# Kernel tuning notes

Measured on AMD Instinct MI355X. Metric: run time of the kernel, lower is better.

Reference implementation:

```python
import jax, jax.numpy as jnp
import numpy as np

B, S, CIN = 16384, 24, 10
NH, DK, DM = 16, 8, 256
DV = DM // NH  # 16
EPS = 1e-5
T_POS = 1000.0


def _ln(x, g, b):
    mu = jnp.mean(x, axis=-1, keepdims=True)
    var = jnp.mean((x - mu) ** 2, axis=-1, keepdims=True)
    return (x - mu) * jax.lax.rsqrt(var + EPS) * g + b


def _bn(x, g, b, m, v):
    # eval-mode BatchNorm1d over channel (last) dim
    return (x - m) * jax.lax.rsqrt(v + EPS) * g + b


def setup_inputs() -> dict:
    key = jax.random.key(0)
    ks = jax.random.split(key, 16)
    x = jax.random.normal(ks[0], (B, S, CIN + 1), dtype=jnp.float32)
    pos = jax.random.uniform(ks[1], (B, S), dtype=jnp.float32) * 365.0
    x = x.at[:, :, 0].set(pos)
    w = lambda k, shp, s=0.05: (jax.random.normal(k, shp, dtype=jnp.float32) * s)
    d = {
        'x': x,
        'ln1_g': jnp.ones((CIN,), jnp.float32), 'ln1_b': jnp.zeros((CIN,), jnp.float32),
        'conv_w': w(ks[2], (DM, CIN)), 'conv_b': jnp.zeros((DM,), jnp.float32),
        'bn1_g': jnp.ones((DM,), jnp.float32), 'bn1_b': jnp.zeros((DM,), jnp.float32),
        'bn1_m': jnp.zeros((DM,), jnp.float32), 'bn1_v': jnp.ones((DM,), jnp.float32),
        'Q': w(ks[3], (NH, DK), float(np.sqrt(2.0 / DK))),
        'Wk': w(ks[4], (NH * DK, DM), float(np.sqrt(2.0 / DK))), 'bk': jnp.zeros((NH * DK,), jnp.float32),
        'W1': w(ks[5], (128, 256)), 'b1': jnp.zeros((128,), jnp.float32),
        'bn2_g': jnp.ones((128,), jnp.float32), 'bn2_b': jnp.zeros((128,), jnp.float32),
        'bn2_m': jnp.zeros((128,), jnp.float32), 'bn2_v': jnp.ones((128,), jnp.float32),
        'oln_g': jnp.ones((128,), jnp.float32), 'oln_b': jnp.zeros((128,), jnp.float32),
        'Wd1': w(ks[6], (64, 128)), 'bd1': jnp.zeros((64,), jnp.float32),
        'bnd1_g': jnp.ones((64,), jnp.float32), 'bnd1_b': jnp.zeros((64,), jnp.float32),
        'bnd1_m': jnp.zeros((64,), jnp.float32), 'bnd1_v': jnp.ones((64,), jnp.float32),
        'Wd2': w(ks[7], (32, 64)), 'bd2': jnp.zeros((32,), jnp.float32),
        'bnd2_g': jnp.ones((32,), jnp.float32), 'bnd2_b': jnp.zeros((32,), jnp.float32),
        'bnd2_m': jnp.zeros((32,), jnp.float32), 'bnd2_v': jnp.ones((32,), jnp.float32),
        'Wd3': w(ks[8], (20, 32)), 'bd3': jnp.zeros((20,), jnp.float32),
    }
    return d


def reference(x, ln1_g, ln1_b, conv_w, conv_b, bn1_g, bn1_b, bn1_m, bn1_v,
              Q, Wk, bk, W1, b1, bn2_g, bn2_b, bn2_m, bn2_v, oln_g, oln_b,
              Wd1, bd1, bnd1_g, bnd1_b, bnd1_m, bnd1_v,
              Wd2, bd2, bnd2_g, bnd2_b, bnd2_m, bnd2_v, Wd3, bd3):
    pos = x[:, :, 0]            # (B, S) positions
    feat = x[:, :, 1:]          # (B, S, CIN)
    feat = _ln(feat, ln1_g, ln1_b)
    # inconv: 1x1 Conv1d == per-timestep Linear, then eval BatchNorm1d over channels
    h = jnp.einsum('bsc,dc->bsd', feat, conv_w) + conv_b
    h = _bn(h, bn1_g, bn1_b, bn1_m, bn1_v)
    # sinusoid positional encoding, interleaved sin/cos
    div = jnp.exp(jnp.arange(0, DM, 2, dtype=jnp.float32) * (-np.log(T_POS) / DM))  # (DM/2,)
    ang = pos[:, :, None] * div                                   # (B, S, DM/2)
    pe = jnp.stack([jnp.sin(ang), jnp.cos(ang)], axis=-1).reshape(pos.shape[0], pos.shape[1], DM)
    e = h + pe                                                    # (B, S, DM)
    # LTAE multi-head attention with shared learned query
    k = jnp.einsum('bsd,hkd->bshk', e, Wk.reshape(NH, DK, DM)) + bk.reshape(NH, DK)
    logits = jnp.einsum('hk,bshk->bhs', Q, k) / np.sqrt(DK)
    attn = jax.nn.softmax(logits, axis=-1)                        # (B, NH, S); dropout=eval
    v = e.reshape(e.shape[0], e.shape[1], NH, DV)                 # head-chunked values
    o = jnp.einsum('bhs,bshc->bhc', attn, v).reshape(e.shape[0], NH * DV)  # (B, 256)
    # MLP3: Linear(256,128) + BN + ReLU, then dropout(eval) + LayerNorm
    m = jax.nn.relu(_bn(o @ W1.T + b1, bn2_g, bn2_b, bn2_m, bn2_v))
    m = _ln(m, oln_g, oln_b)
    # decoder: [128,64,32,20]
    d1 = jax.nn.relu(_bn(m @ Wd1.T + bd1, bnd1_g, bnd1_b, bnd1_m, bnd1_v))
    d2 = jax.nn.relu(_bn(d1 @ Wd2.T + bd2, bnd2_g, bnd2_b, bnd2_m, bnd2_v))
    out = d2 @ Wd3.T + bd3                                        # (B, 20)
    return out
```

## Files before the change

kernel.cpp:

```cpp
#include <hip/hip_runtime.h>
#include <hip/hip_bf16.h>


typedef __attribute__((ext_vector_type(8))) short bf16x8;
typedef __attribute__((ext_vector_type(4))) float f32x4;

#define EPS 1e-5f
#define INV_SQRT8 0.35355339059327373f
#define KDIV (-0.07785768972392256f)
#define INV2PI 0.15915494309189535f
#define LOG2E 1.4426950408889634f

__device__ __forceinline__ unsigned short f2bf(float f){
  union { float f; unsigned u; } v; v.f = f;
  unsigned r = v.u + 0x7FFFu + ((v.u >> 16) & 1u);
  return (unsigned short)(r >> 16);
}
__device__ __forceinline__ float bf2f(unsigned short h){
  union { unsigned u; float f; } v; v.u = ((unsigned)h) << 16; return v.f;
}
__device__ __forceinline__ unsigned pk2bf(float lo, float hi){
  __hip_bfloat162 h2 = __float22bfloat162_rn(make_float2(lo, hi));
  return *reinterpret_cast<unsigned*>(&h2);
}
__device__ __forceinline__ float sin_rev(float rev){
  rev -= floorf(rev);
  return __builtin_amdgcn_sinf(rev);
}

__global__ __launch_bounds__(256) void k0_pre(
    const float* __restrict__ conv_w, const float* __restrict__ conv_b,
    const float* __restrict__ bn1_g, const float* __restrict__ bn1_b,
    const float* __restrict__ bn1_m, const float* __restrict__ bn1_v,
    const float* __restrict__ Q, const float* __restrict__ Wk,
    const float* __restrict__ bk,
    const float* __restrict__ W1, const float* __restrict__ b1,
    const float* __restrict__ bn2_g, const float* __restrict__ bn2_b,
    const float* __restrict__ bn2_m, const float* __restrict__ bn2_v,
    const float* __restrict__ oln_g, const float* __restrict__ oln_b,
    const float* __restrict__ Wd1, const float* __restrict__ bd1,
    const float* __restrict__ bnd1_g, const float* __restrict__ bnd1_b,
    const float* __restrict__ bnd1_m, const float* __restrict__ bnd1_v,
    const float* __restrict__ Wd2, const float* __restrict__ bd2,
    const float* __restrict__ bnd2_g, const float* __restrict__ bnd2_b,
    const float* __restrict__ bnd2_m, const float* __restrict__ bnd2_v,
    const float* __restrict__ Wd3,
    unsigned short* __restrict__ wqF, unsigned short* __restrict__ w1F,
    unsigned short* __restrict__ wd1F, unsigned short* __restrict__ wd2F,
    unsigned short* __restrict__ wd3F,
    float* __restrict__ convwT, float* __restrict__ convbE,
    float* __restrict__ biasq, float* __restrict__ b1E,
    float* __restrict__ bd1E, float* __restrict__ bd2E)
{
  __shared__ float redL[256];
  const int t = threadIdx.x;
  const int bid = blockIdx.x;

  if (bid < 64){
    for (int e = bid*512 + t; e < bid*512 + 512; e += 256){
      int j = e & 7, lj = (e >> 3) & 63, kc = (e >> 9) & 7, nt = (e >> 12) & 7;
      int n = nt*16 + (lj & 15);
      int k = kc*32 + ((lj >> 4) << 3) + j;
      float s2 = bn2_g[n] * rsqrtf(bn2_v[n] + EPS);
      w1F[e] = f2bf(W1[n*256 + k] * s2);
    }
  } else if (bid < 68){
    int base = (bid - 64)*2048;
    #pragma unroll 4
    for (int it = 0; it < 8; ++it){
      int e = base + it*256 + t;
      int j = e & 7, lj = (e >> 3) & 63, kc = (e >> 9) & 3, nt = (e >> 11) & 3;
      int n = nt*16 + (lj & 15);
      int k = kc*32 + ((lj >> 4) << 3) + j;
      float sd = bnd1_g[n] * rsqrtf(bnd1_v[n] + EPS);
      wd1F[e] = f2bf(Wd1[n*128 + k] * sd * oln_g[k]);
    }
  } else if (bid == 68){
    #pragma unroll 4
    for (int it = 0; it < 8; ++it){
      int e = it*256 + t;
      int j = e & 7, lj = (e >> 3) & 63, kc = (e >> 9) & 1, nt = (e >> 10) & 1;
      int n = nt*16 + (lj & 15);
      int k = kc*32 + ((lj >> 4) << 3) + j;
      float sd = bnd2_g[n] * rsqrtf(bnd2_v[n] + EPS);
      wd2F[e] = f2bf(Wd2[n*64 + k] * sd);
    }
  } else if (bid == 69){
    #pragma unroll
    for (int it = 0; it < 4; ++it){
      int e = it*256 + t;
      int j = e & 7, lj = (e >> 3) & 63, nt = (e >> 9) & 1;
      int n = nt*16 + (lj & 15);
      int k = ((lj >> 4) << 3) + j;
      float v = (n < 20) ? Wd3[n*32 + k] : 0.f;
      wd3F[e] = f2bf(v);
    }
  } else if (bid == 70){
    #pragma unroll 4
    for (int it = 0; it < 16; ++it){
      int e = it*256 + t;
      int j = e & 7, lj = (e >> 3) & 63, kc = (e >> 9) & 7;
      int h = lj & 15;
      int dd = kc*32 + ((lj >> 4) << 3) + j;
      float acc = 0.f;
      #pragma unroll
      for (int kk = 0; kk < 8; ++kk)
        acc += Q[h*8+kk] * Wk[(h*8+kk)*256 + dd];
      wqF[e] = f2bf(acc * INV_SQRT8);
    }
  } else if (bid == 71){
    __shared__ float wqL[16*256];
    __shared__ float coefL[256*12];
    __shared__ float QL[128];
    __shared__ float bkL[128];
    wqF[4096 + t] = 0; wqF[4096 + 256 + t] = 0;
    if (t < 128){ QL[t] = Q[t]; bkL[t] = bk[t]; }
    __syncthreads();
    {
      const int d = t;
      float s1 = bn1_g[d] * rsqrtf(bn1_v[d] + EPS);
      #pragma unroll
      for (int c = 0; c < 10; ++c) coefL[d*12 + c] = conv_w[d*10 + c] * s1;
      coefL[d*12 + 10] = conv_b[d]*s1 + bn1_b[d] - bn1_m[d]*s1;
      coefL[d*12 + 11] = 0.f;
      #pragma unroll 4
      for (int h = 0; h < 16; ++h){
        float acc = 0.f;
        #pragma unroll
        for (int kk = 0; kk < 8; ++kk)
          acc += QL[h*8+kk] * Wk[(h*8+kk)*256 + d];
        wqL[h*256 + d] = acc;
      }
    }
    __syncthreads();
    if (t < 176){
      int h = t / 11, cc = t - h*11;
      const float* wq = wqL + h*256;
      float acc = 0.f;
      #pragma unroll 4
      for (int d2 = 0; d2 < 256; ++d2)
        acc += coefL[d2*12 + cc] * wq[d2];
      acc *= INV_SQRT8;
      if (cc < 10){
        int lane = (cc < 8) ? h : (16 + h);
        int j = cc & 7;
        wqF[4096 + lane*8 + j] = f2bf(acc);
      } else {
        float qb = 0.f;
        #pragma unroll
        for (int kk = 0; kk < 8; ++kk) qb += QL[h*8+kk]*bkL[h*8+kk];
        biasq[h] = acc + qb * INV_SQRT8;
      }
    }
  } else if (bid == 72){
    #pragma unroll
    for (int it = 0; it < 10; ++it){
      int e = it*256 + t;
      int c = e >> 8, d = e & 255;
      float s1 = bn1_g[d] * rsqrtf(bn1_v[d] + EPS);
      convwT[e] = conv_w[d*10 + c] * s1;
    }
  } else if (bid == 73){
    {
      int d = t;
      float s1 = bn1_g[d] * rsqrtf(bn1_v[d] + EPS);
      convbE[d] = conv_b[d]*s1 + bn1_b[d] - bn1_m[d]*s1;
    }
    if (t < 128){
      float s2 = bn2_g[t] * rsqrtf(bn2_v[t] + EPS);
      b1E[t] = b1[t]*s2 + bn2_b[t] - bn2_m[t]*s2;
    }
    if (t < 32){
      float sd = bnd2_g[t] * rsqrtf(bnd2_v[t] + EPS);
      bd2E[t] = bd2[t]*sd + bnd2_b[t] - bnd2_m[t]*sd;
    }
  } else {
    int n = t >> 2, si = t & 3;
    float acc = 0.f;
    #pragma unroll 8
    for (int i2 = 0; i2 < 32; ++i2){
      int i = si*32 + i2;
      acc += oln_b[i] * Wd1[n*128 + i];
    }
    redL[t] = acc;
    __syncthreads();
    if (t < 64){
      float sd = bnd1_g[t] * rsqrtf(bnd1_v[t] + EPS);
      float a = redL[4*t] + redL[4*t+1] + redL[4*t+2] + redL[4*t+3];
      bd1E[t] = bd1[t]*sd + bnd1_b[t] - bnd1_m[t]*sd + a*sd;
    }
  }
}

__global__ __launch_bounds__(256, 4) void k1_attn(
    const float* __restrict__ x, const float* __restrict__ ln1_g,
    const float* __restrict__ ln1_b,
    const unsigned short* __restrict__ wqF, const float* __restrict__ convwT,
    const float* __restrict__ convbE, const float* __restrict__ biasq,
    unsigned short* __restrict__ o_ws)
{
  __shared__ unsigned short featn[48*32];
  __shared__ float posL[48];
  __shared__ float divL[128];
  __shared__ unsigned short peF[1536*8];
  __shared__ float attnF[2*16*28];
  __shared__ float gL[2*16*12];

  const int t = threadIdx.x;
  const int b0 = blockIdx.x * 2;

  if (t < 128) divL[t] = exp2f((float)t * KDIV) * INV2PI;

  if (t < 48){
    int bb = t >= 24; int s = t - bb*24;
    const float* xr = x + ((size_t)(b0+bb)*24 + s)*11;
    float f[10]; float mu = 0.f;
    #pragma unroll
    for (int c = 0; c < 10; ++c){ f[c] = xr[1+c]; mu += f[c]; }
    posL[t] = xr[0];
    mu *= 0.1f;
    float var = 0.f;
    #pragma unroll
    for (int c = 0; c < 10; ++c){ float dv = f[c]-mu; var += dv*dv; }
    var *= 0.1f;
    float rs = rsqrtf(var + EPS);
    float fn[10];
    #pragma unroll
    for (int c = 0; c < 10; ++c) fn[c] = (f[c]-mu)*rs*ln1_g[c] + ln1_b[c];
    #pragma unroll
    for (int q = 0; q < 5; ++q)
      *(unsigned*)(featn + t*32 + 2*q) = pk2bf(fn[2*q], fn[2*q+1]);
    #pragma unroll
    for (int z = 0; z < 11; ++z)
      *(unsigned*)(featn + t*32 + 10 + 2*z) = 0u;
  }
  __syncthreads();

  {
    const int w = t >> 6, l = t & 63;
    const int g = (l >> 4) & 3, rlo = l & 15;
    #pragma unroll
    for (int it = 0; it < 6; ++it){
      int combo = it*4 + w;
      int mt = combo >> 3, kc = combo & 7;
      int row = mt*16 + rlo;
      int run = kc*4 + g;
      float p = posL[row];
      unsigned pk[4];
      #pragma unroll
      for (int q = 0; q < 4; ++q){
        float dv = divL[run*4 + q];
        float ang = p * dv;
        float fr = ang - floorf(ang);
        float sv = __builtin_amdgcn_sinf(fr);
        float cv = __builtin_amdgcn_cosf(fr);
        pk[q] = pk2bf(sv, cv);
      }
      uint4* dst = (uint4*)(peF + ((size_t)((mt*8+kc)*64 + l))*8);
      *dst = make_uint4(pk[0], pk[1], pk[2], pk[3]);
    }
  }

  unsigned peT[24];
  {
    const int d = t;
    float dv = divL[d >> 1];
    float ofs = (d & 1) ? 0.25f : 0.f;
    #pragma unroll
    for (int r2 = 0; r2 < 24; ++r2){
      float v0 = sin_rev(posL[2*r2]   * dv + ofs);
      float v1 = sin_rev(posL[2*r2+1] * dv + ofs);
      peT[r2] = pk2bf(v0, v1);
    }
  }
  __syncthreads();

  {
    const int w = t >> 6, l = t & 63;
    if (w < 3){
      const int mt = w;
      f32x4 acc = {0.f,0.f,0.f,0.f};
      #pragma unroll
      for (int kc = 0; kc < 8; ++kc){
        bf16x8 a = *(const bf16x8*)(peF + ((size_t)((mt*8+kc)*64 + l))*8);
        bf16x8 b = *(const bf16x8*)(wqF + ((size_t)(kc*64 + l))*8);
        acc = __builtin_amdgcn_mfma_f32_16x16x32_bf16(a, b, acc, 0, 0, 0);
      }
      {
        bf16x8 a = *(const bf16x8*)(featn + (mt*16 + (l & 15))*32 + ((l>>4)<<3));
        bf16x8 b = *(const bf16x8*)(wqF + ((size_t)(8*64 + l))*8);
        acc = __builtin_amdgcn_mfma_f32_16x16x32_bf16(a, b, acc, 0, 0, 0);
      }
      const int h = l & 15;
      float bq = biasq[h];
      #pragma unroll
      for (int reg = 0; reg < 4; ++reg){
        int row = mt*16 + ((l>>4)<<2) + reg;
        int bb = row >= 24; int s = row - bb*24;
        attnF[(bb*16+h)*28 + s] = acc[reg] + bq;
      }
    }
  }
  __syncthreads();

  if (t < 32){
    float* L = attnF + t*28;
    float mx = -1e30f;
    for (int s = 0; s < 24; ++s) mx = fmaxf(mx, L[s]);
    float sum = 0.f;
    for (int s = 0; s < 24; ++s){
      float p = exp2f((L[s]-mx)*LOG2E); L[s] = p; sum += p;
    }
    float inv = 1.f / sum;
    for (int s = 0; s < 24; ++s) L[s] *= inv;
  }
  __syncthreads();

  if (t < 160){
    int bb = t / 80; int rem = t - bb*80;
    int h = rem / 5, c = rem - h*5;
    const float* A = attnF + (bb*16+h)*28;
    float g0 = 0.f, g1 = 0.f;
    for (int s = 0; s < 24; ++s){
      float a = A[s];
      const unsigned short* fr = featn + (bb*24+s)*32;
      g0 += a * bf2f(fr[c]);
      g1 += a * bf2f(fr[c+5]);
    }
    gL[(bb*16+h)*12 + c]     = g0;
    gL[(bb*16+h)*12 + c + 5] = g1;
  }
  __syncthreads();

  {
    const int d = t, h = d >> 4;
    float cw[10];
    #pragma unroll
    for (int c = 0; c < 10; ++c) cw[c] = convwT[c*256 + d];
    float cb = convbE[d];
    #pragma unroll
    for (int bb = 0; bb < 2; ++bb){
      float o = cb;
      const float* gp = gL + (bb*16+h)*12;
      #pragma unroll
      for (int c = 0; c < 10; ++c) o += cw[c]*gp[c];
      const float* A = attnF + (bb*16+h)*28;
      #pragma unroll
      for (int rr = 0; rr < 12; ++rr){
        unsigned pv = peT[bb*12 + rr];
        o += A[2*rr]   * bf2f((unsigned short)(pv & 0xFFFFu));
        o += A[2*rr+1] * bf2f((unsigned short)(pv >> 16));
      }
      o_ws[(size_t)(b0+bb)*256 + d] = f2bf(o);
    }
  }
}

__global__ __launch_bounds__(256, 2) void k2_mlp(
    const unsigned short* __restrict__ o_ws,
    const unsigned short* __restrict__ w1F, const float* __restrict__ b1E,
    const unsigned short* __restrict__ wd1F, const float* __restrict__ bd1E,
    const unsigned short* __restrict__ wd2F, const float* __restrict__ bd2E,
    const unsigned short* __restrict__ wd3F, const float* __restrict__ bd3,
    float* __restrict__ out)
{
  __shared__ float mL[32*132];
  __shared__ unsigned short mh[32*136];
  __shared__ unsigned short d1L[32*72];
  __shared__ unsigned short d2L[32*40];
  __shared__ float redL[128];
  __shared__ float stats[64];

  const int t = threadIdx.x;
  const int w = t >> 6, l = t & 63;
  const size_t rowBase = (size_t)blockIdx.x * 32;
  const int g8  = (l >> 4) << 3;
  const int c15 = l & 15;

  {
    f32x4 acc[2][2];
    #pragma unroll
    for (int i = 0; i < 2; ++i)
      #pragma unroll
      for (int j = 0; j < 2; ++j){ f32x4 z = {0.f,0.f,0.f,0.f}; acc[i][j] = z; }
    #pragma unroll
    for (int kc = 0; kc < 8; ++kc){
      bf16x8 a0 = *(const bf16x8*)(o_ws + (rowBase + c15)*256      + kc*32 + g8);
      bf16x8 a1 = *(const bf16x8*)(o_ws + (rowBase + 16 + c15)*256 + kc*32 + g8);
      #pragma unroll
      for (int n2 = 0; n2 < 2; ++n2){
        int nt = 2*w + n2;
        bf16x8 b = *(const bf16x8*)(w1F + ((size_t)((nt*8+kc)*64 + l))*8);
        acc[0][n2] = __builtin_amdgcn_mfma_f32_16x16x32_bf16(a0, b, acc[0][n2], 0,0,0);
        acc[1][n2] = __builtin_amdgcn_mfma_f32_16x16x32_bf16(a1, b, acc[1][n2], 0,0,0);
      }
    }
    #pragma unroll
    for (int n2 = 0; n2 < 2; ++n2){
      int col = (2*w + n2)*16 + c15;
      float be = b1E[col];
      #pragma unroll
      for (int mt = 0; mt < 2; ++mt)
        #pragma unroll
        for (int reg = 0; reg < 4; ++reg){
          int row = mt*16 + ((l>>4)<<2) + reg;
          mL[row*132 + col] = fmaxf(acc[mt][n2][reg] + be, 0.f);
        }
    }
  }
  __syncthreads();

  if (t < 64){
    const float* R = mL + (t>>1)*132 + (t&1)*64;
    float s = 0.f, q = 0.f;
    for (int k = 0; k < 64; ++k){ float v = R[k]; s += v; q += v*v; }
    redL[t*2] = s; redL[t*2+1] = q;
  }
  __syncthreads();
  if (t < 32){
    float s = redL[4*t] + redL[4*t+2];
    float q = redL[4*t+1] + redL[4*t+3];
    float mu = s * (1.f/128.f);
    float var = q * (1.f/128.f) - mu*mu;
    stats[2*t] = mu; stats[2*t+1] = rsqrtf(var + EPS);
  }
  __syncthreads();

  for (int u = t; u < 512; u += 256){
    int r = u >> 4, run = u & 15;
    float mu = stats[2*r], rs = stats[2*r+1];
    const float* R = mL + r*132 + run*8;
    unsigned pk[4];
    #pragma unroll
    for (int q = 0; q < 4; ++q)
      pk[q] = pk2bf((R[2*q]-mu)*rs, (R[2*q+1]-mu)*rs);
    *(uint4*)(mh + r*136 + run*8) = make_uint4(pk[0], pk[1], pk[2], pk[3]);
  }
  __syncthreads();

  {
    const int nt = w;
    f32x4 acc[2];
    { f32x4 z = {0.f,0.f,0.f,0.f}; acc[0] = z; acc[1] = z; }
    #pragma unroll
    for (int kc = 0; kc < 4; ++kc){
      bf16x8 b = *(const bf16x8*)(wd1F + ((size_t)((nt*4+kc)*64 + l))*8);
      #pragma unroll
      for (int mt = 0; mt < 2; ++mt){
        bf16x8 a = *(const bf16x8*)(mh + (mt*16 + c15)*136 + kc*32 + g8);
        acc[mt] = __builtin_amdgcn_mfma_f32_16x16x32_bf16(a, b, acc[mt], 0,0,0);
      }
    }
    int col = nt*16 + c15;
    float be = bd1E[col];
    #pragma unroll
    for (int mt = 0; mt < 2; ++mt)
      #pragma unroll
      for (int reg = 0; reg < 4; ++reg){
        int row = mt*16 + ((l>>4)<<2) + reg;
        d1L[row*72 + col] = f2bf(fmaxf(acc[mt][reg] + be, 0.f));
      }
  }
  __syncthreads();

  {
    const int mt = w >> 1, nt = w & 1;
    f32x4 acc = {0.f,0.f,0.f,0.f};
    #pragma unroll
    for (int kc = 0; kc < 2; ++kc){
      bf16x8 a = *(const bf16x8*)(d1L + (mt*16 + c15)*72 + kc*32 + g8);
      bf16x8 b = *(const bf16x8*)(wd2F + ((size_t)((nt*2+kc)*64 + l))*8);
      acc = __builtin_amdgcn_mfma_f32_16x16x32_bf16(a, b, acc, 0,0,0);
    }
    int col = nt*16 + c15;
    float be = bd2E[col];
    #pragma unroll
    for (int reg = 0; reg < 4; ++reg){
      int row = mt*16 + ((l>>4)<<2) + reg;
      d2L[row*40 + col] = f2bf(fmaxf(acc[reg] + be, 0.f));
    }
  }
  __syncthreads();

  {
    const int mt = w >> 1, nt = w & 1;
    bf16x8 a = *(const bf16x8*)(d2L + (mt*16 + c15)*40 + g8);
    bf16x8 b = *(const bf16x8*)(wd3F + ((size_t)(nt*64 + l))*8);
    f32x4 acc = {0.f,0.f,0.f,0.f};
    acc = __builtin_amdgcn_mfma_f32_16x16x32_bf16(a, b, acc, 0,0,0);
    int col = nt*16 + c15;
    if (col < 20){
      float be = bd3[col];
      #pragma unroll
      for (int reg = 0; reg < 4; ++reg){
        int row = mt*16 + ((l>>4)<<2) + reg;
        out[(rowBase + row)*20 + col] = acc[reg] + be;
      }
    }
  }
}

extern "C" void kernel_launch(void* const* d_in, const int* in_sizes, int n_in,
                              void* d_out, int out_size, void* d_ws, size_t ws_size,
                              hipStream_t stream)
{
  (void)in_sizes; (void)n_in; (void)out_size; (void)ws_size;
  const float* x      = (const float*)d_in[0];
  const float* ln1_g  = (const float*)d_in[1];
  const float* ln1_b  = (const float*)d_in[2];
  const float* conv_w = (const float*)d_in[3];
  const float* conv_b = (const float*)d_in[4];
  const float* bn1_g  = (const float*)d_in[5];
  const float* bn1_b  = (const float*)d_in[6];
  const float* bn1_m  = (const float*)d_in[7];
  const float* bn1_v  = (const float*)d_in[8];
  const float* Q      = (const float*)d_in[9];
  const float* Wk     = (const float*)d_in[10];
  const float* bk     = (const float*)d_in[11];
  const float* W1     = (const float*)d_in[12];
  const float* b1     = (const float*)d_in[13];
  const float* bn2_g  = (const float*)d_in[14];
  const float* bn2_b  = (const float*)d_in[15];
  const float* bn2_m  = (const float*)d_in[16];
  const float* bn2_v  = (const float*)d_in[17];
  const float* oln_g  = (const float*)d_in[18];
  const float* oln_b  = (const float*)d_in[19];
  const float* Wd1    = (const float*)d_in[20];
  const float* bd1    = (const float*)d_in[21];
  const float* bnd1_g = (const float*)d_in[22];
  const float* bnd1_b = (const float*)d_in[23];
  const float* bnd1_m = (const float*)d_in[24];
  const float* bnd1_v = (const float*)d_in[25];
  const float* Wd2    = (const float*)d_in[26];
  const float* bd2    = (const float*)d_in[27];
  const float* bnd2_g = (const float*)d_in[28];
  const float* bnd2_b = (const float*)d_in[29];
  const float* bnd2_m = (const float*)d_in[30];
  const float* bnd2_v = (const float*)d_in[31];
  const float* Wd3    = (const float*)d_in[32];
  const float* bd3    = (const float*)d_in[33];

  char* ws = (char*)d_ws;
  unsigned short* wqF  = (unsigned short*)(ws + 0);
  unsigned short* w1F  = (unsigned short*)(ws + 9216);
  unsigned short* wd1F = (unsigned short*)(ws + 74752);
  unsigned short* wd2F = (unsigned short*)(ws + 91136);
  unsigned short* wd3F = (unsigned short*)(ws + 95232);
  float* convwT = (float*)(ws + 97280);
  float* convbE = (float*)(ws + 107520);
  float* biasq  = (float*)(ws + 108544);
  float* b1E    = (float*)(ws + 108608);
  float* bd1E   = (float*)(ws + 109120);
  float* bd2E   = (float*)(ws + 109376);
  unsigned short* o_ws = (unsigned short*)(ws + 109568);

  hipLaunchKernelGGL(k0_pre, dim3(75), dim3(256), 0, stream,
      conv_w, conv_b, bn1_g, bn1_b, bn1_m, bn1_v, Q, Wk, bk,
      W1, b1, bn2_g, bn2_b, bn2_m, bn2_v, oln_g, oln_b,
      Wd1, bd1, bnd1_g, bnd1_b, bnd1_m, bnd1_v,
      Wd2, bd2, bnd2_g, bnd2_b, bnd2_m, bnd2_v, Wd3,
      wqF, w1F, wd1F, wd2F, wd3F, convwT, convbE, biasq, b1E, bd1E, bd2E);

  hipLaunchKernelGGL(k1_attn, dim3(8192), dim3(256), 0, stream,
      x, ln1_g, ln1_b, wqF, convwT, convbE, biasq, o_ws);

  hipLaunchKernelGGL(k2_mlp, dim3(512), dim3(256), 0, stream,
      o_ws, w1F, b1E, wd1F, bd1E, wd2F, bd2E, wd3F, bd3, (float*)d_out);
}
```

Before: 206.9 us.

## Store PE row-major in LDS, drop per-thread PE recompute, halve MLP tile

The attention kernel now writes the sinusoidal positional encoding once into a row-major LDS array. The MFMA A-operand and the per-channel value reduction both read from that array, so the second register-resident sin/cos recomputation (peT) is gone. The feature buffer shrinks to 16 columns, with a zero buffer feeding the unused MFMA lanes, and several LDS arrays are aliased. The MLP kernel processes 16 rows per block instead of 32 across twice as many blocks, with a higher occupancy hint. This trades transcendental recompute for extra LDS traffic and possible bank conflicts on strided reads.

```diff
diff --git a/kernel.cpp b/kernel.cpp
--- a/kernel.cpp
+++ b/kernel.cpp
@@ -22,10 +22,6 @@
 __device__ __forceinline__ unsigned pk2bf(float lo, float hi){
   __hip_bfloat162 h2 = __float22bfloat162_rn(make_float2(lo, hi));
   return *reinterpret_cast<unsigned*>(&h2);
-}
-__device__ __forceinline__ float sin_rev(float rev){
-  rev -= floorf(rev);
-  return __builtin_amdgcn_sinf(rev);
 }
 
 __global__ __launch_bounds__(256) void k0_pre(
@@ -199,17 +195,21 @@
     const float* __restrict__ convbE, const float* __restrict__ biasq,
     unsigned short* __restrict__ o_ws)
 {
-  __shared__ unsigned short featn[48*32];
-  __shared__ float posL[48];
-  __shared__ float divL[128];
-  __shared__ unsigned short peF[1536*8];
+  __shared__ unsigned short peR[48*264];
+  __shared__ unsigned short featn[48*16];
   __shared__ float attnF[2*16*28];
-  __shared__ float gL[2*16*12];
+  __shared__ float shmix[384];
+  __shared__ __align__(16) unsigned short zeroB[8];
+  float* posL = shmix;
+  float* divL = shmix + 64;
+  float* gL   = shmix;
 
   const int t = threadIdx.x;
   const int b0 = blockIdx.x * 2;
+  const int w = t >> 6, l = t & 63;
 
   if (t < 128) divL[t] = exp2f((float)t * KDIV) * INV2PI;
+  if (t < 8) zeroB[t] = 0;
 
   if (t < 48){
     int bb = t >= 24; int s = t - bb*24;
@@ -229,15 +229,14 @@
     for (int c = 0; c < 10; ++c) fn[c] = (f[c]-mu)*rs*ln1_g[c] + ln1_b[c];
     #pragma unroll
     for (int q = 0; q < 5; ++q)
-      *(unsigned*)(featn + t*32 + 2*q) = pk2bf(fn[2*q], fn[2*q+1]);
-    #pragma unroll
-    for (int z = 0; z < 11; ++z)
-      *(unsigned*)(featn + t*32 + 10 + 2*z) = 0u;
+      *(unsigned*)(featn + t*16 + 2*q) = pk2bf(fn[2*q], fn[2*q+1]);
+    #pragma unroll
+    for (int z = 0; z < 3; ++z)
+      *(unsigned*)(featn + t*16 + 10 + 2*z) = 0u;
   }
   __syncthreads();
 
   {
-    const int w = t >> 6, l = t & 63;
     const int g = (l >> 4) & 3, rlo = l & 15;
     #pragma unroll
     for (int it = 0; it < 6; ++it){
@@ -256,46 +255,34 @@
         float cv = __builtin_amdgcn_cosf(fr);
         pk[q] = pk2bf(sv, cv);
       }
-      uint4* dst = (uint4*)(peF + ((size_t)((mt*8+kc)*64 + l))*8);
-      *dst = make_uint4(pk[0], pk[1], pk[2], pk[3]);
-    }
-  }
-
-  unsigned peT[24];
+      *(uint4*)(peR + row*264 + run*8) = make_uint4(pk[0], pk[1], pk[2], pk[3]);
+    }
+  }
+  __syncthreads();
+
   {
-    const int d = t;
-    float dv = divL[d >> 1];
-    float ofs = (d & 1) ? 0.25f : 0.f;
-    #pragma unroll
-    for (int r2 = 0; r2 < 24; ++r2){
-      float v0 = sin_rev(posL[2*r2]   * dv + ofs);
-      float v1 = sin_rev(posL[2*r2+1] * dv + ofs);
-      peT[r2] = pk2bf(v0, v1);
-    }
-  }
-  __syncthreads();
-
-  {
-    const int w = t >> 6, l = t & 63;
     if (w < 3){
       const int mt = w;
+      const int m = l & 15, g = l >> 4;
       f32x4 acc = {0.f,0.f,0.f,0.f};
       #pragma unroll
       for (int kc = 0; kc < 8; ++kc){
-        bf16x8 a = *(const bf16x8*)(peF + ((size_t)((mt*8+kc)*64 + l))*8);
+        bf16x8 a = *(const bf16x8*)(peR + (mt*16 + m)*264 + kc*32 + g*8);
         bf16x8 b = *(const bf16x8*)(wqF + ((size_t)(kc*64 + l))*8);
         acc = __builtin_amdgcn_mfma_f32_16x16x32_bf16(a, b, acc, 0, 0, 0);
       }
       {
-        bf16x8 a = *(const bf16x8*)(featn + (mt*16 + (l & 15))*32 + ((l>>4)<<3));
+        const unsigned short* ap = (g < 2) ? (featn + (mt*16 + m)*16 + g*8)
+                                           : zeroB;
+        bf16x8 a = *(const bf16x8*)ap;
         bf16x8 b = *(const bf16x8*)(wqF + ((size_t)(8*64 + l))*8);
         acc = __builtin_amdgcn_mfma_f32_16x16x32_bf16(a, b, acc, 0, 0, 0);
       }
-      const int h = l & 15;
+      const int h = m;
       float bq = biasq[h];
       #pragma unroll
       for (int reg = 0; reg < 4; ++reg){
-        int row = mt*16 + ((l>>4)<<2) + reg;
+        int row = mt*16 + g*4 + reg;
         int bb = row >= 24; int s = row - bb*24;
         attnF[(bb*16+h)*28 + s] = acc[reg] + bq;
       }
@@ -323,7 +310,7 @@
     float g0 = 0.f, g1 = 0.f;
     for (int s = 0; s < 24; ++s){
       float a = A[s];
-      const unsigned short* fr = featn + (bb*24+s)*32;
+      const unsigned short* fr = featn + (bb*24+s)*16;
       g0 += a * bf2f(fr[c]);
       g1 += a * bf2f(fr[c+5]);
     }
@@ -345,18 +332,16 @@
       #pragma unroll
       for (int c = 0; c < 10; ++c) o += cw[c]*gp[c];
       const float* A = attnF + (bb*16+h)*28;
-      #pragma unroll
-      for (int rr = 0; rr < 12; ++rr){
-        unsigned pv = peT[bb*12 + rr];
-        o += A[2*rr]   * bf2f((unsigned short)(pv & 0xFFFFu));
-        o += A[2*rr+1] * bf2f((unsigned short)(pv >> 16));
-      }
+      const unsigned short* pr = peR + (bb*24)*264 + d;
+      #pragma unroll
+      for (int s = 0; s < 24; ++s)
+        o += A[s] * bf2f(pr[s*264]);
       o_ws[(size_t)(b0+bb)*256 + d] = f2bf(o);
     }
   }
 }
 
-__global__ __launch_bounds__(256, 2) void k2_mlp(
+__global__ __launch_bounds__(256, 4) void k2_mlp(
     const unsigned short* __restrict__ o_ws,
     const unsigned short* __restrict__ w1F, const float* __restrict__ b1E,
     const unsigned short* __restrict__ wd1F, const float* __restrict__ bd1E,
@@ -364,35 +349,30 @@
     const unsigned short* __restrict__ wd3F, const float* __restrict__ bd3,
     float* __restrict__ out)
 {
-  __shared__ float mL[32*132];
-  __shared__ unsigned short mh[32*136];
-  __shared__ unsigned short d1L[32*72];
-  __shared__ unsigned short d2L[32*40];
-  __shared__ float redL[128];
-  __shared__ float stats[64];
+  __shared__ float mL[16*132];
+  __shared__ unsigned short mh[16*136];
+  __shared__ unsigned short d1L[16*72];
+  __shared__ unsigned short d2L[16*40];
+  __shared__ float redL[64];
+  __shared__ float stats[32];
 
   const int t = threadIdx.x;
   const int w = t >> 6, l = t & 63;
-  const size_t rowBase = (size_t)blockIdx.x * 32;
+  const size_t rowBase = (size_t)blockIdx.x * 16;
   const int g8  = (l >> 4) << 3;
   const int c15 = l & 15;
 
   {
-    f32x4 acc[2][2];
-    #pragma unroll
-    for (int i = 0; i < 2; ++i)
-      #pragma unroll
-      for (int j = 0; j < 2; ++j){ f32x4 z = {0.f,0.f,0.f,0.f}; acc[i][j] = z; }
+    f32x4 acc[2];
+    { f32x4 z = {0.f,0.f,0.f,0.f}; acc[0] = z; acc[1] = z; }
     #pragma unroll
     for (int kc = 0; kc < 8; ++kc){
-      bf16x8 a0 = *(const bf16x8*)(o_ws + (rowBase + c15)*256      + kc*32 + g8);
-      bf16x8 a1 = *(const bf16x8*)(o_ws + (rowBase + 16 + c15)*256 + kc*32 + g8);
+      bf16x8 a = *(const bf16x8*)(o_ws + (rowBase + c15)*256 + kc*32 + g8);
       #pragma unroll
       for (int n2 = 0; n2 < 2; ++n2){
         int nt = 2*w + n2;
         bf16x8 b = *(const bf16x8*)(w1F + ((size_t)((nt*8+kc)*64 + l))*8);
-        acc[0][n2] = __builtin_amdgcn_mfma_f32_16x16x32_bf16(a0, b, acc[0][n2], 0,0,0);
-        acc[1][n2] = __builtin_amdgcn_mfma_f32_16x16x32_bf16(a1, b, acc[1][n2], 0,0,0);
+        acc[n2] = __builtin_amdgcn_mfma_f32_16x16x32_bf16(a, b, acc[n2], 0,0,0);
       }
     }
     #pragma unroll
@@ -400,24 +380,22 @@
       int col = (2*w + n2)*16 + c15;
       float be = b1E[col];
       #pragma unroll
-      for (int mt = 0; mt < 2; ++mt)
-        #pragma unroll
-        for (int reg = 0; reg < 4; ++reg){
-          int row = mt*16 + ((l>>4)<<2) + reg;
-          mL[row*132 + col] = fmaxf(acc[mt][n2][reg] + be, 0.f);
-        }
-    }
-  }
-  __syncthreads();
-
-  if (t < 64){
+      for (int reg = 0; reg < 4; ++reg){
+        int row = ((l>>4)<<2) + reg;
+        mL[row*132 + col] = fmaxf(acc[n2][reg] + be, 0.f);
+      }
+    }
+  }
+  __syncthreads();
+
+  if (t < 32){
     const float* R = mL + (t>>1)*132 + (t&1)*64;
     float s = 0.f, q = 0.f;
     for (int k = 0; k < 64; ++k){ float v = R[k]; s += v; q += v*v; }
     redL[t*2] = s; redL[t*2+1] = q;
   }
   __syncthreads();
-  if (t < 32){
+  if (t < 16){
     float s = redL[4*t] + redL[4*t+2];
     float q = redL[4*t+1] + redL[4*t+3];
     float mu = s * (1.f/128.f);
@@ -426,8 +404,8 @@
   }
   __syncthreads();
 
-  for (int u = t; u < 512; u += 256){
-    int r = u >> 4, run = u & 15;
+  {
+    int r = t >> 4, run = t & 15;
     float mu = stats[2*r], rs = stats[2*r+1];
     const float* R = mL + r*132 + run*8;
     unsigned pk[4];
@@ -440,35 +418,29 @@
 
   {
     const int nt = w;
-    f32x4 acc[2];
-    { f32x4 z = {0.f,0.f,0.f,0.f}; acc[0] = z; acc[1] = z; }
+    f32x4 acc = {0.f,0.f,0.f,0.f};
     #pragma unroll
     for (int kc = 0; kc < 4; ++kc){
       bf16x8 b = *(const bf16x8*)(wd1F + ((size_t)((nt*4+kc)*64 + l))*8);
-      #pragma unroll
-      for (int mt = 0; mt < 2; ++mt){
-        bf16x8 a = *(const bf16x8*)(mh + (mt*16 + c15)*136 + kc*32 + g8);
-        acc[mt] = __builtin_amdgcn_mfma_f32_16x16x32_bf16(a, b, acc[mt], 0,0,0);
-      }
+      bf16x8 a = *(const bf16x8*)(mh + c15*136 + kc*32 + g8);
+      acc = __builtin_amdgcn_mfma_f32_16x16x32_bf16(a, b, acc, 0,0,0);
     }
     int col = nt*16 + c15;
     float be = bd1E[col];
     #pragma unroll
-    for (int mt = 0; mt < 2; ++mt)
-      #pragma unroll
-      for (int reg = 0; reg < 4; ++reg){
-        int row = mt*16 + ((l>>4)<<2) + reg;
-        d1L[row*72 + col] = f2bf(fmaxf(acc[mt][reg] + be, 0.f));
-      }
-  }
-  __syncthreads();
-
-  {
-    const int mt = w >> 1, nt = w & 1;
+    for (int reg = 0; reg < 4; ++reg){
+      int row = ((l>>4)<<2) + reg;
+      d1L[row*72 + col] = f2bf(fmaxf(acc[reg] + be, 0.f));
+    }
+  }
+  __syncthreads();
+
+  if (w < 2){
+    const int nt = w;
     f32x4 acc = {0.f,0.f,0.f,0.f};
     #pragma unroll
     for (int kc = 0; kc < 2; ++kc){
-      bf16x8 a = *(const bf16x8*)(d1L + (mt*16 + c15)*72 + kc*32 + g8);
+      bf16x8 a = *(const bf16x8*)(d1L + c15*72 + kc*32 + g8);
       bf16x8 b = *(const bf16x8*)(wd2F + ((size_t)((nt*2+kc)*64 + l))*8);
       acc = __builtin_amdgcn_mfma_f32_16x16x32_bf16(a, b, acc, 0,0,0);
     }
@@ -476,15 +448,15 @@
     float be = bd2E[col];
     #pragma unroll
     for (int reg = 0; reg < 4; ++reg){
-      int row = mt*16 + ((l>>4)<<2) + reg;
+      int row = ((l>>4)<<2) + reg;
       d2L[row*40 + col] = f2bf(fmaxf(acc[reg] + be, 0.f));
     }
   }
   __syncthreads();
 
-  {
-    const int mt = w >> 1, nt = w & 1;
-    bf16x8 a = *(const bf16x8*)(d2L + (mt*16 + c15)*40 + g8);
+  if (w < 2){
+    const int nt = w;
+    bf16x8 a = *(const bf16x8*)(d2L + c15*40 + g8);
     bf16x8 b = *(const bf16x8*)(wd3F + ((size_t)(nt*64 + l))*8);
     f32x4 acc = {0.f,0.f,0.f,0.f};
     acc = __builtin_amdgcn_mfma_f32_16x16x32_bf16(a, b, acc, 0,0,0);
@@ -493,7 +465,7 @@
       float be = bd3[col];
       #pragma unroll
       for (int reg = 0; reg < 4; ++reg){
-        int row = mt*16 + ((l>>4)<<2) + reg;
+        int row = ((l>>4)<<2) + reg;
         out[(rowBase + row)*20 + col] = acc[reg] + be;
       }
     }
@@ -564,6 +536,6 @@
   hipLaunchKernelGGL(k1_attn, dim3(8192), dim3(256), 0, stream,
       x, ln1_g, ln1_b, wqF, convwT, convbE, biasq, o_ws);
 
-  hipLaunchKernelGGL(k2_mlp, dim3(512), dim3(256), 0, stream,
+  hipLaunchKernelGGL(k2_mlp, dim3(1024), dim3(256), 0, stream,
       o_ws, w1F, b1E, wd1F, bd1E, wd2F, bd2E, wd3F, bd3, (float*)d_out);
 }
```

Result: faster. 193.5 us (-6.5%).
